# Optimization experiments

Measured on AMD Instinct MI355X. Metric: run time of the kernel, lower is better.

Reference implementation:

```python
import jax, jax.numpy as jnp
import numpy as np

B, L, D = 256, 256, 128          # batch, max_len, embedding_dim
H = W = 16                       # H=int(sqrt(L)), W=L//H
N, CBD = 128, 1024               # embedding_num, code_book_dim = N*8 = D*8
BETA = 0.25
BN_EPS = 1e-3                    # tf.layers.batch_normalization default


def _conv(x, w, b):
    return jax.lax.conv_general_dilated(x, w, (1, 1), 'VALID',
        dimension_numbers=('NHWC', 'HWIO', 'NHWC')) + b


def _convT(x, w, b):
    return jax.lax.conv_transpose(x, w, (1, 1), 'VALID',
        dimension_numbers=('NHWC', 'HWIO', 'NHWC')) + b


def _bn(x, g, b):
    # inference-mode BN with moving_mean=0, moving_var=1 (tf.layers default training=False)
    return g * (x * (1.0 / np.sqrt(1.0 + BN_EPS))) + b


def setup_inputs() -> dict:
    key = jax.random.key(0)
    ks = jax.random.split(key, 24)
    rn = lambda k, s, sc=0.05: (jax.random.normal(k, s, dtype=jnp.float32) * sc)
    inp = {
        'x': jax.random.normal(ks[0], (B, L, D), dtype=jnp.float32),
        'mask': jnp.ones((B, L), dtype=jnp.float32),
        'code_book': jax.random.normal(ks[1], (N, CBD), dtype=jnp.float32),
        # encoder: conv2d k=2 valid, channels D -> 2D -> 4D -> 8D
        'ew1': rn(ks[2], (2, 2, D, 2 * D)), 'eb1': jnp.zeros((2 * D,), jnp.float32),
        'eg1': jnp.ones((2 * D,), jnp.float32), 'ebt1': jnp.zeros((2 * D,), jnp.float32),
        'ew2': rn(ks[3], (2, 2, 2 * D, 4 * D)), 'eb2': jnp.zeros((4 * D,), jnp.float32),
        'eg2': jnp.ones((4 * D,), jnp.float32), 'ebt2': jnp.zeros((4 * D,), jnp.float32),
        'ew3': rn(ks[4], (2, 2, 4 * D, 8 * D)), 'eb3': jnp.zeros((8 * D,), jnp.float32),
        # decoder: conv2d_transpose k=2 valid, channels 8D -> 4D -> 2D -> D
        'dw1': rn(ks[5], (2, 2, 8 * D, 4 * D)), 'db1': jnp.zeros((4 * D,), jnp.float32),
        'dg1': jnp.ones((4 * D,), jnp.float32), 'dbt1': jnp.zeros((4 * D,), jnp.float32),
        'dw2': rn(ks[6], (2, 2, 4 * D, 2 * D)), 'db2': jnp.zeros((2 * D,), jnp.float32),
        'dg2': jnp.ones((2 * D,), jnp.float32), 'dbt2': jnp.zeros((2 * D,), jnp.float32),
        'dw3': rn(ks[7], (2, 2, 2 * D, D)), 'db3': jnp.zeros((D,), jnp.float32),
    }
    return inp


def reference(x, mask, code_book,
              ew1, eb1, eg1, ebt1, ew2, eb2, eg2, ebt2, ew3, eb3,
              dw1, db1, dg1, dbt1, dw2, db2, dg2, dbt2, dw3, db3):
    # ---- encoder (conv branch) ----
    xi = x.reshape(-1, H, W, D)                                   # [B,16,16,D]
    h = jax.nn.relu(_bn(_conv(xi, ew1, eb1), eg1, ebt1))          # [B,15,15,2D]
    h = jax.nn.relu(_bn(_conv(h, ew2, eb2), eg2, ebt2))           # [B,14,14,4D]
    x_encode = _conv(h, ew3, eb3)                                 # [B,13,13,8D]

    # ---- VQ codebook lookup (get_quantized) ----
    flat = x_encode.reshape(-1, CBD)                              # [B*169, CBD]
    dist = (jnp.sum(flat ** 2, axis=1, keepdims=True)
            + jnp.sum(code_book ** 2, axis=1)
            - 2.0 * flat @ code_book.T)                           # [B*169, N]
    idx = jnp.argmin(dist, axis=1)
    quantized = code_book[idx].reshape(x_encode.shape)            # gather == one_hot @ code_book

    # ---- straight-through + decoder ----
    ste = x_encode + jax.lax.stop_gradient(quantized - x_encode)
    h = jax.nn.relu(_bn(_convT(ste, dw1, db1), dg1, dbt1))        # [B,14,14,4D]
    h = jax.nn.relu(_bn(_convT(h, dw2, db2), dg2, dbt2))          # [B,15,15,2D]
    vq = _convT(h, dw3, db3)                                      # [B,16,16,D]
    vq_x = vq.reshape(-1, L, D)

    vq_mean = jnp.sum(vq_x, axis=1) / jnp.sum(mask, axis=-1, keepdims=True)

    recon = jnp.mean((x - vq_x) ** 2)
    vq_l = jnp.mean((quantized - jax.lax.stop_gradient(x_encode)) ** 2)
    commit = jnp.mean((x_encode - jax.lax.stop_gradient(quantized)) ** 2)
    vqvae_loss = recon + vq_l + BETA * commit
    return (vq_mean, vq_x, x_encode, quantized, vqvae_loss)
```

## Files before the change

kernel.cpp:

```cpp
#include <hip/hip_runtime.h>
#include <math.h>

typedef float f4 __attribute__((ext_vector_type(4)));
typedef short s8 __attribute__((ext_vector_type(8)));

#define WS_FLOATS 66000000L
__device__ float g_fallback[WS_FLOATS];

__device__ __forceinline__ f4 ldg4(const float* p) { return *(const f4*)p; }

__device__ __forceinline__ unsigned short bfr(float x) {
    unsigned int u = __float_as_uint(x);
    u += 0x7fffu + ((u >> 16) & 1u);
    return (unsigned short)(u >> 16);
}
__device__ __forceinline__ float bff(unsigned short h) {
    return __uint_as_float(((unsigned int)h) << 16);
}
__device__ __forceinline__ s8 z8() { s8 z = {0,0,0,0,0,0,0,0}; return z; }

__device__ __forceinline__ void split8(const f4& x0, const f4& x1, s8& hi, s8& lo) {
#pragma unroll
    for (int e = 0; e < 4; ++e) {
        unsigned short h0 = bfr(x0[e]);
        hi[e] = (short)h0; lo[e] = (short)bfr(x0[e] - bff(h0));
        unsigned short h1 = bfr(x1[e]);
        hi[e + 4] = (short)h1; lo[e + 4] = (short)bfr(x1[e] - bff(h1));
    }
}

template<int SPLIT, int ASRC, int EPI, int OUTF>
__global__ __launch_bounds__(256, 2)
void mfma_conv(const void* __restrict__ aHi, const void* __restrict__ aLo,
               const short* __restrict__ wHi, const short* __restrict__ wLo,
               const float* __restrict__ bias, const float* __restrict__ gamma,
               const float* __restrict__ beta,
               void* __restrict__ oHi, void* __restrict__ oLo,
               int* __restrict__ idxo,
               int IH, int IW, int Cin, int cinShift, int OHOW, int OW,
               int N, int K, int off, int ntShift, float bns)
{
    constexpr int PL = 128 * 64;
    __shared__ short smem[2 * SPLIT * PL];
    short* Ah = smem;
    short* Al = smem + PL;
    short* Bh = smem + SPLIT * PL;
    short* Bl = smem + SPLIT * PL + PL;

    const int tid = threadIdx.x;
    const int lane = tid & 63, wid = tid >> 6;
    const int fr = lane & 15, fq = lane >> 4;
    const int wm = (wid >> 1) * 64, wn = (wid & 1) * 64;

    int m0, n0;
    {
        const int nwg = gridDim.x;
        const int bid = blockIdx.x;
        const int q = nwg >> 3, r = nwg & 7;
        const int xcd = bid & 7, c = bid >> 3;
        const int wg = (xcd < r ? xcd * (q + 1) : r * (q + 1) + (xcd - r) * q) + c;
        const int NTm1 = (1 << ntShift) - 1;
        m0 = (wg >> ntShift) * 128;
        n0 = (wg & NTm1) * 128;
    }

    const int sr = tid >> 1;
    const int skh = (tid & 1) << 5;

    long tapOff[4]; bool tv[4];
    {
        int m = m0 + sr;
        int b = m / OHOW; int rem = m - b * OHOW;
        int oi = rem / OW; int oj = rem - oi * OW;
#pragma unroll
        for (int t = 0; t < 4; ++t) {
            int ii = oi + (t >> 1) + off, jj = oj + (t & 1) + off;
            bool v = (ii >= 0) && (ii < IH) && (jj >= 0) && (jj < IW);
            tv[t] = v;
            tapOff[t] = ((long)b * IH + (v ? ii : 0)) * IW + (v ? jj : 0);
        }
    }

    f4 acc[4][4];
#pragma unroll
    for (int a = 0; a < 4; ++a)
#pragma unroll
        for (int b = 0; b < 4; ++b) acc[a][b] = (f4){0.f, 0.f, 0.f, 0.f};

    const short* wHrow = wHi + (long)(n0 + sr) * K;
    const short* wLrow = (SPLIT == 2) ? (wLo + (long)(n0 + sr) * K) : nullptr;

    const int swzW = (sr & 7) << 3;
    const int sbase = sr * 64;

    s8 rah[4], ral[4], rbh[4], rbl[4];
    f4 rax0[4], rax1[4];

    auto LOADREGS = [&](int kc) {
        const int kk = kc + skh;
        const int t = kk >> cinShift;
        const int ci = kk & (Cin - 1);
        const bool v = tv[t];
        if (ASRC == 0) {
            const float* p = (const float*)aHi + tapOff[t] * Cin + ci;
#pragma unroll
            for (int q = 0; q < 4; ++q) {
                rax0[q] = v ? ldg4(p + 8 * q) : (f4){0.f,0.f,0.f,0.f};
                rax1[q] = v ? ldg4(p + 8 * q + 4) : (f4){0.f,0.f,0.f,0.f};
            }
        } else if (ASRC == 1) {
            const short* ph = (const short*)aHi + tapOff[t] * Cin + ci;
            const short* pl = (const short*)aLo + tapOff[t] * Cin + ci;
#pragma unroll
            for (int q = 0; q < 4; ++q) {
                rah[q] = v ? *(const s8*)(ph + 8 * q) : z8();
                ral[q] = v ? *(const s8*)(pl + 8 * q) : z8();
            }
        } else {
            const short* ph = (const short*)aHi + tapOff[t] * Cin + ci;
#pragma unroll
            for (int q = 0; q < 4; ++q) rah[q] = v ? *(const s8*)(ph + 8 * q) : z8();
        }
#pragma unroll
        for (int q = 0; q < 4; ++q) {
            rbh[q] = *(const s8*)(wHrow + kc + skh + 8 * q);
            if (SPLIT == 2) rbl[q] = *(const s8*)(wLrow + kc + skh + 8 * q);
        }
    };

    auto STORE = [&]() {
        if (ASRC == 0) {
#pragma unroll
            for (int q = 0; q < 4; ++q) split8(rax0[q], rax1[q], rah[q], ral[q]);
        }
#pragma unroll
        for (int q = 0; q < 4; ++q) {
            int kx = (skh + 8 * q) ^ swzW;
            *(s8*)&Ah[sbase + kx] = rah[q];
            if (SPLIT == 2) *(s8*)&Al[sbase + kx] = ral[q];
            *(s8*)&Bh[sbase + kx] = rbh[q];
            if (SPLIT == 2) *(s8*)&Bl[sbase + kx] = rbl[q];
        }
    };

    LOADREGS(0);
    for (int kc = 0; kc < K; kc += 64) {
        __syncthreads();
        STORE();
        __syncthreads();
        if (kc + 64 < K) LOADREGS(kc + 64);

        __builtin_amdgcn_s_setprio(1);
#pragma unroll
        for (int ks = 0; ks < 2; ++ks) {
            const int colk = ks * 32 + fq * 8;
            s8 afh[4], afl[4], bfh[4], bfl[4];
#pragma unroll
            for (int mf = 0; mf < 4; ++mf) {
                int ar = wm + mf * 16 + fr;
                int ai = ar * 64 + (colk ^ ((ar & 7) << 3));
                afh[mf] = *(const s8*)&Ah[ai];
                if (SPLIT == 2) afl[mf] = *(const s8*)&Al[ai];
            }
#pragma unroll
            for (int nf = 0; nf < 4; ++nf) {
                int br = wn + nf * 16 + fr;
                int bi2 = br * 64 + (colk ^ ((br & 7) << 3));
                bfh[nf] = *(const s8*)&Bh[bi2];
                if (SPLIT == 2) bfl[nf] = *(const s8*)&Bl[bi2];
            }
#pragma unroll
            for (int mf = 0; mf < 4; ++mf)
#pragma unroll
                for (int nf = 0; nf < 4; ++nf) {
                    acc[mf][nf] = __builtin_amdgcn_mfma_f32_16x16x32_bf16(
                        afh[mf], bfh[nf], acc[mf][nf], 0, 0, 0);
                    if (SPLIT == 2) {
                        acc[mf][nf] = __builtin_amdgcn_mfma_f32_16x16x32_bf16(
                            afh[mf], bfl[nf], acc[mf][nf], 0, 0, 0);
                        acc[mf][nf] = __builtin_amdgcn_mfma_f32_16x16x32_bf16(
                            afl[mf], bfh[nf], acc[mf][nf], 0, 0, 0);
                    }
                }
        }
        __builtin_amdgcn_s_setprio(0);
    }

    if (EPI == 2) {
        __syncthreads();
        float* pbv = (float*)smem;
        int*   piv = (int*)((float*)smem + 256);
        float cnv[4];
#pragma unroll
        for (int nf = 0; nf < 4; ++nf) cnv[nf] = bias[n0 + wn + nf * 16 + fr];
#pragma unroll
        for (int mf = 0; mf < 4; ++mf)
#pragma unroll
            for (int j = 0; j < 4; ++j) {
                float best = 3.4e38f; int bi = 0;
#pragma unroll
                for (int nf = 0; nf < 4; ++nf) {
                    float d = cnv[nf] - 2.0f * acc[mf][nf][j];
                    int col = wn + nf * 16 + fr;
                    if (d < best) { best = d; bi = col; }
                }
#pragma unroll
                for (int sh = 1; sh <= 8; sh <<= 1) {
                    float ov = __shfl_xor(best, sh, 64);
                    int ob = __shfl_xor(bi, sh, 64);
                    if (ov < best || (ov == best && ob < bi)) { best = ov; bi = ob; }
                }
                if (fr == 0) {
                    int r = wm + mf * 16 + fq * 4 + j;
                    pbv[(wid & 1) * 128 + r] = best;
                    piv[(wid & 1) * 128 + r] = bi;
                }
            }
        __syncthreads();
        if (tid < 128) {
            float b0 = pbv[tid], b1 = pbv[128 + tid];
            int i0 = piv[tid], i1 = piv[128 + tid];
            idxo[m0 + tid] = (b1 < b0) ? i1 : i0;
        }
        return;
    }

    float bi[4], ga[4], be[4];
#pragma unroll
    for (int nf = 0; nf < 4; ++nf) {
        int col = n0 + wn + nf * 16 + fr;
        bi[nf] = bias[col];
        if (EPI == 1) { ga[nf] = gamma[col]; be[nf] = beta[col]; }
    }
#pragma unroll
    for (int mf = 0; mf < 4; ++mf)
#pragma unroll
        for (int j = 0; j < 4; ++j) {
            long gm = m0 + wm + mf * 16 + fq * 4 + j;
#pragma unroll
            for (int nf = 0; nf < 4; ++nf) {
                int col = n0 + wn + nf * 16 + fr;
                float vv = acc[mf][nf][j] + bi[nf];
                if (EPI == 1) {
                    vv = ga[nf] * (vv * bns) + be[nf];
                    vv = fmaxf(vv, 0.f);
                }
                long o = gm * (long)N + col;
                if (OUTF == 0) {
                    ((float*)oHi)[o] = vv;
                } else if (OUTF == 2) {
                    ((short*)oHi)[o] = (short)bfr(vv);
                } else {
                    unsigned short h = bfr(vv);
                    ((short*)oHi)[o] = (short)h;
                    ((short*)oLo)[o] = (short)bfr(vv - bff(h));
                }
            }
        }
}

__global__ void prep_all(const float* __restrict__ ew1, const float* __restrict__ ew2,
                         const float* __restrict__ ew3, const float* __restrict__ dw1,
                         const float* __restrict__ dw2, const float* __restrict__ dw3,
                         const float* __restrict__ cb,
                         short* __restrict__ ewt1h, short* __restrict__ ewt1l,
                         short* __restrict__ ewt2h, short* __restrict__ ewt2l,
                         short* __restrict__ ewt3h,
                         short* __restrict__ dwt1Th, short* __restrict__ dwt1Tl,
                         short* __restrict__ dwt2h, short* __restrict__ dwt3h,
                         short* __restrict__ cbh, short* __restrict__ cbl,
                         float* __restrict__ zbuf)
{
    int b = blockIdx.x;
    int t = threadIdx.x;
    if (b < 512) {
        int i = b * 256 + t; int n = i >> 9, k = i & 511;
        float x = ew1[(long)k * 256 + n]; unsigned short h = bfr(x);
        ewt1h[i] = (short)h; ewt1l[i] = (short)bfr(x - bff(h));
    } else if (b < 2560) {
        int i = (b - 512) * 256 + t; int n = i >> 10, k = i & 1023;
        float x = ew2[(long)k * 512 + n]; unsigned short h = bfr(x);
        ewt2h[i] = (short)h; ewt2l[i] = (short)bfr(x - bff(h));
    } else if (b < 10752) {
        int i = (b - 2560) * 256 + t; int n = i >> 11, k = i & 2047;
        ewt3h[i] = (short)bfr(ew3[(long)k * 1024 + n]);
    } else if (b < 18944) {
        int i = (b - 10752) * 256 + t; int Np = i >> 10, co = i & 1023;
        int tt = Np >> 9, nn = Np & 511;
        float x = dw1[((long)(tt * 1024 + co)) * 512 + nn]; unsigned short h = bfr(x);
        dwt1Th[i] = (short)h; dwt1Tl[i] = (short)bfr(x - bff(h));
    } else if (b < 20992) {
        int i = (b - 18944) * 256 + t; int n = i >> 11, k = i & 2047;
        dwt2h[i] = (short)bfr(dw2[(long)k * 256 + n]);
    } else if (b < 21504) {
        int i = (b - 20992) * 256 + t; int n = i >> 10, k = i & 1023;
        dwt3h[i] = (short)bfr(dw3[(long)k * 128 + n]);
    } else if (b < 22016) {
        int i = (b - 21504) * 256 + t;
        float x = cb[i]; unsigned short h = bfr(x);
        cbh[i] = (short)h; cbl[i] = (short)bfr(x - bff(h));
    } else {
        int i = (b - 22016) * 256 + t; if (i < 2048) zbuf[i] = 0.f;
    }
}

__global__ void wsplitT(const float* __restrict__ p1, short* __restrict__ hi,
                        short* __restrict__ lo)
{
    int i = blockIdx.x * 256 + threadIdx.x;
    if (i >= 262144) return;
    int n = i >> 11, k = i & 2047;
    float x = p1[(long)k * 128 + n];
    unsigned short h = bfr(x);
    hi[i] = (short)h;
    lo[i] = (short)bfr(x - bff(h));
}

__global__ void code_bias(const float* __restrict__ cb, const float* __restrict__ eb3,
                          float* __restrict__ bias2)
{
    int c = blockIdx.x * 4 + (threadIdx.x >> 6);
    int lane = threadIdx.x & 63;
    if (c >= 128) return;
    const f4* p = (const f4*)(cb + (long)c * 1024);
    const f4* e = (const f4*)eb3;
    float s2 = 0.f, su = 0.f;
#pragma unroll
    for (int q = 0; q < 4; ++q) {
        f4 v = p[q * 64 + lane];
        f4 w = e[q * 64 + lane];
        s2 += (v[0]*v[0] + v[1]*v[1]) + (v[2]*v[2] + v[3]*v[3]);
        su += (v[0]*w[0] + v[1]*w[1]) + (v[2]*w[2] + v[3]*w[3]);
    }
#pragma unroll
    for (int sh = 32; sh; sh >>= 1) {
        s2 += __shfl_xor(s2, sh, 64);
        su += __shfl_xor(su, sh, 64);
    }
    if (lane == 0) bias2[c] = s2 - 2.f * su;
}

__global__ __launch_bounds__(256)
void d1_gather(const float* __restrict__ CD, const int* __restrict__ idx,
               const float* __restrict__ db1, const float* __restrict__ dg1,
               const float* __restrict__ dbt1, short* __restrict__ out, float bns)
{
    int m = blockIdx.x * 4 + (threadIdx.x >> 6);
    int lane = threadIdx.x & 63;
    if (m >= 50176) return;
    int b = m / 196, rem = m - b * 196;
    int oi = rem / 14, oj = rem - oi * 14;
    float2 acc[4];
#pragma unroll
    for (int q = 0; q < 4; ++q) acc[q] = make_float2(0.f, 0.f);
#pragma unroll
    for (int t = 0; t < 4; ++t) {
        int ii = oi - 1 + (t >> 1), jj = oj - 1 + (t & 1);
        if (ii >= 0 && ii < 13 && jj >= 0 && jj < 13) {
            int c = idx[(b * 13 + ii) * 13 + jj];
            const float2* p = (const float2*)(CD + ((long)c * 2048 + t * 512));
#pragma unroll
            for (int q = 0; q < 4; ++q) {
                float2 v = p[lane + 64 * q];
                acc[q].x += v.x; acc[q].y += v.y;
            }
        }
    }
#pragma unroll
    for (int q = 0; q < 4; ++q) {
        int n = 2 * (lane + 64 * q);
        float v0 = fmaxf(dg1[n]     * ((acc[q].x + db1[n])     * bns) + dbt1[n],     0.f);
        float v1 = fmaxf(dg1[n + 1] * ((acc[q].y + db1[n + 1]) * bns) + dbt1[n + 1], 0.f);
        short2 s2v;
        s2v.x = (short)bfr(v0); s2v.y = (short)bfr(v1);
        ((short2*)out)[(long)m * 256 + lane + 64 * q] = s2v;
    }
}

__global__ __launch_bounds__(256)
void gather_sq(const float* __restrict__ cb, const int* __restrict__ idx,
               const float* __restrict__ xe, float* __restrict__ q,
               double* __restrict__ part, int rows)
{
    __shared__ double red[256];
    double s = 0.0;
    for (int m = blockIdx.x; m < rows; m += gridDim.x) {
        int c = idx[m];
        const f4* src = (const f4*)(cb + (long)c * 1024);
        const f4* xs  = (const f4*)(xe + (long)m * 1024);
        f4* dst = (f4*)(q + (long)m * 1024);
        f4 v = src[threadIdx.x];
        f4 xv = xs[threadIdx.x];
        dst[threadIdx.x] = v;
        f4 d = v - xv;
        s += ((double)d[0]*d[0] + (double)d[1]*d[1]) + ((double)d[2]*d[2] + (double)d[3]*d[3]);
    }
    red[threadIdx.x] = s; __syncthreads();
    for (int h = 128; h; h >>= 1) {
        if (threadIdx.x < h) red[threadIdx.x] += red[threadIdx.x + h];
        __syncthreads();
    }
    if (threadIdx.x == 0) part[blockIdx.x] = red[0];
}

__global__ void sqdiff_partial(const float* __restrict__ a, const float* __restrict__ b,
                               double* __restrict__ part, long n4)
{
    __shared__ double red[256];
    long i = (long)blockIdx.x * blockDim.x + threadIdx.x;
    long stride = (long)gridDim.x * blockDim.x;
    const f4* A = (const f4*)a;
    const f4* B = (const f4*)b;
    f4 s = (f4){0.f, 0.f, 0.f, 0.f};
    for (; i < n4; i += stride) {
        f4 d = A[i] - B[i];
        s += d * d;
    }
    double t = ((double)s[0] + s[1]) + ((double)s[2] + s[3]);
    red[threadIdx.x] = t;
    __syncthreads();
    for (int h = 128; h; h >>= 1) {
        if (threadIdx.x < h) red[threadIdx.x] += red[threadIdx.x + h];
        __syncthreads();
    }
    if (threadIdx.x == 0) part[blockIdx.x] = red[0];
}

__global__ void finalize_k(const double* __restrict__ pa, int na,
                           const double* __restrict__ pb, int nb,
                           float* __restrict__ loss)
{
    __shared__ double red[256];
    int t = threadIdx.x;
    double sa = 0;
    for (int i = t; i < na; i += 256) sa += pa[i];
    red[t] = sa; __syncthreads();
    for (int h = 128; h; h >>= 1) { if (t < h) red[t] += red[t + h]; __syncthreads(); }
    double SA = red[0];
    __syncthreads();
    double sb = 0;
    for (int i = t; i < nb; i += 256) sb += pb[i];
    red[t] = sb; __syncthreads();
    for (int h = 128; h; h >>= 1) { if (t < h) red[t] += red[t + h]; __syncthreads(); }
    if (t == 0) {
        double recon = SA / 8388608.0;
        double vql = red[0] / 44302336.0;
        loss[0] = (float)(recon + 1.25 * vql);
    }
}

__global__ void vq_mean_k(const float* __restrict__ vqx, const float* __restrict__ mask,
                          float* __restrict__ o)
{
    __shared__ float red[128];
    int b = blockIdx.x;
    int d = threadIdx.x;
    red[d] = mask[b * 256 + d] + mask[b * 256 + 128 + d];
    __syncthreads();
    for (int h = 64; h; h >>= 1) { if (d < h) red[d] += red[d + h]; __syncthreads(); }
    float msum = red[0];
    const float* p = vqx + (long)b * 256 * 128 + d;
    float s = 0.f;
    for (int l = 0; l < 256; ++l) s += p[l * 128];
    o[b * 128 + d] = s / msum;
}

extern "C" void kernel_launch(void* const* d_in, const int* in_sizes, int n_in,
                              void* d_out, int out_size, void* d_ws, size_t ws_size,
                              hipStream_t stream)
{
    const float* x    = (const float*)d_in[0];
    const float* mask = (const float*)d_in[1];
    const float* cb   = (const float*)d_in[2];
    const float* ew1 = (const float*)d_in[3];
    const float* eb1 = (const float*)d_in[4];
    const float* eg1 = (const float*)d_in[5];
    const float* ebt1= (const float*)d_in[6];
    const float* ew2 = (const float*)d_in[7];
    const float* eb2 = (const float*)d_in[8];
    const float* eg2 = (const float*)d_in[9];
    const float* ebt2= (const float*)d_in[10];
    const float* ew3 = (const float*)d_in[11];
    const float* eb3 = (const float*)d_in[12];
    const float* dw1 = (const float*)d_in[13];
    const float* db1 = (const float*)d_in[14];
    const float* dg1 = (const float*)d_in[15];
    const float* dbt1= (const float*)d_in[16];
    const float* dw2 = (const float*)d_in[17];
    const float* db2 = (const float*)d_in[18];
    const float* dg2 = (const float*)d_in[19];
    const float* dbt2= (const float*)d_in[20];
    const float* dw3 = (const float*)d_in[21];
    const float* db3 = (const float*)d_in[22];

    float* out = (float*)d_out;
    float* o_vqmean = out;
    float* o_vqx    = out + 32768;
    float* o_xe     = out + 8421376;
    float* o_q      = out + 52723712;
    float* o_loss   = out + 97026048;

    float* base;
    if (ws_size >= (size_t)WS_FLOATS * 4) {
        base = (float*)d_ws;
    } else {
        void* p = nullptr;
        hipGetSymbolAddress(&p, HIP_SYMBOL(g_fallback));
        base = (float*)p;
    }

    float* cur = base;
    short* h1h = (short*)cur; cur += 7372800;
    short* h1l = (short*)cur; cur += 7372800;
    short* h2h = (short*)cur; cur += 12845056;
    short* h2l = (short*)cur; cur += 12845056;
    short* d1o = (short*)cur; cur += 12845056;
    short* d2o = (short*)cur; cur += 7372800;
    short* ewt1h = (short*)cur; cur += 65536;
    short* ewt1l = (short*)cur; cur += 65536;
    short* ewt2h = (short*)cur; cur += 262144;
    short* ewt2l = (short*)cur; cur += 262144;
    short* ewt3h = (short*)cur; cur += 1048576;
    short* dwt1Th = (short*)cur; cur += 1048576;
    short* dwt1Tl = (short*)cur; cur += 1048576;
    short* dwt2h = (short*)cur; cur += 262144;
    short* dwt3h = (short*)cur; cur += 65536;
    short* cbh   = (short*)cur; cur += 65536;
    short* cbl   = (short*)cur; cur += 65536;
    float* P1raw = cur; cur += 262144;
    short* wvh   = (short*)cur; cur += 131072;
    short* wvl   = (short*)cur; cur += 131072;
    float* CDt   = cur; cur += 262144;
    float* bias2 = cur; cur += 128;
    float* zbuf  = cur; cur += 2048;
    int* idxb = (int*)cur; cur += 43264;
    double* pa = (double*)cur; cur += 4096;
    double* pq = (double*)cur; cur += 4096;

    const float bns = (float)(1.0 / sqrt(1.0 + 1e-3));

    prep_all<<<22024, 256, 0, stream>>>(ew1, ew2, ew3, dw1, dw2, dw3, cb,
        ewt1h, ewt1l, ewt2h, ewt2l, ewt3h, dwt1Th, dwt1Tl, dwt2h, dwt3h,
        cbh, cbl, zbuf);
    code_bias<<<32, 256, 0, stream>>>(cb, eb3, bias2);

    mfma_conv<2, 0, 0, 0><<<16, 256, 0, stream>>>(
        ew3, nullptr, cbh, cbl, zbuf, nullptr, nullptr, P1raw, nullptr, nullptr,
        2, 2050, 1024, 10, 2048, 2048, 128, 1024, 0, 0, bns);
    wsplitT<<<1024, 256, 0, stream>>>(P1raw, wvh, wvl);
    mfma_conv<2, 0, 0, 0><<<16, 256, 0, stream>>>(
        cb, nullptr, dwt1Th, dwt1Tl, zbuf, nullptr, nullptr, CDt, nullptr, nullptr,
        2, 130, 1024, 10, 128, 128, 2048, 1024, 0, 4, bns);

    mfma_conv<2, 0, 1, 1><<<900, 256, 0, stream>>>(
        x, nullptr, ewt1h, ewt1l, eb1, eg1, ebt1, h1h, h1l, nullptr,
        16, 16, 128, 7, 225, 15, 256, 512, 0, 1, bns);
    mfma_conv<2, 1, 1, 1><<<1568, 256, 0, stream>>>(
        h1h, h1l, ewt2h, ewt2l, eb2, eg2, ebt2, h2h, h2l, nullptr,
        15, 15, 256, 8, 196, 14, 512, 1024, 0, 2, bns);
    mfma_conv<1, 2, 0, 0><<<2704, 256, 0, stream>>>(
        h2h, nullptr, ewt3h, nullptr, eb3, nullptr, nullptr, o_xe, nullptr, nullptr,
        14, 14, 512, 9, 169, 13, 1024, 2048, 0, 3, bns);

    mfma_conv<2, 1, 2, 0><<<338, 256, 0, stream>>>(
        h2h, h2l, wvh, wvl, bias2, nullptr, nullptr, nullptr, nullptr, idxb,
        14, 14, 512, 9, 169, 13, 128, 2048, 0, 0, bns);
    gather_sq<<<2048, 256, 0, stream>>>(cb, idxb, o_xe, o_q, pq, 43264);

    d1_gather<<<12544, 256, 0, stream>>>(CDt, idxb, db1, dg1, dbt1, d1o, bns);
    mfma_conv<1, 2, 1, 2><<<900, 256, 0, stream>>>(
        d1o, nullptr, dwt2h, nullptr, db2, dg2, dbt2, d2o, nullptr, nullptr,
        14, 14, 512, 9, 225, 15, 256, 2048, -1, 1, bns);
    mfma_conv<1, 2, 0, 0><<<512, 256, 0, stream>>>(
        d2o, nullptr, dwt3h, nullptr, db3, nullptr, nullptr, o_vqx, nullptr, nullptr,
        15, 15, 256, 8, 256, 16, 128, 1024, -1, 0, bns);

    vq_mean_k<<<256, 128, 0, stream>>>(o_vqx, mask, o_vqmean);
    sqdiff_partial<<<1024, 256, 0, stream>>>(x, o_vqx, pa, 2097152L);
    finalize_k<<<1, 256, 0, stream>>>(pa, 1024, pq, 2048, o_loss);
}
```

Measured before the change: 953.9 us.

## Fuse loss reductions into conv epilogues and stream B tiles via global_load_lds

In the SPLIT==1 conv path, the B-tile weights are now loaded straight into double-buffered LDS with global_load_lds and explicit waitcnt/barriers, so they no longer pass through registers. The squared-difference loss, the vq loss (using the argmin distance plus the ||x||^2 sum from the x_encode epilogue) and the vq_mean column sums are computed inside the conv epilogues with atomics. This removes the separate gather_sq, sqdiff_partial and vq_mean passes over large tensors. The cost is atomic contention and a nondeterministic floating-point summation order, and the vq loss is now rebuilt algebraically from distances, which can lose precision through cancellation.

```diff
diff --git a/kernel.cpp b/kernel.cpp
--- a/kernel.cpp
+++ b/kernel.cpp
@@ -37,15 +37,18 @@
                const float* __restrict__ beta,
                void* __restrict__ oHi, void* __restrict__ oLo,
                int* __restrict__ idxo,
+               const float* __restrict__ xref, float* __restrict__ colsum,
+               double* __restrict__ sacc,
                int IH, int IW, int Cin, int cinShift, int OHOW, int OW,
                int N, int K, int off, int ntShift, float bns)
 {
     constexpr int PL = 128 * 64;
-    __shared__ short smem[2 * SPLIT * PL];
+    constexpr int NPL = (SPLIT == 1) ? 3 : 4;
+    __shared__ short smem[NPL * PL];
     short* Ah = smem;
-    short* Al = smem + PL;
-    short* Bh = smem + SPLIT * PL;
-    short* Bl = smem + SPLIT * PL + PL;
+    short* Al  = smem + PL;
+    short* BhS = smem + 2 * PL;
+    short* BlS = smem + 3 * PL;
 
     const int tid = threadIdx.x;
     const int lane = tid & 63, wid = tid >> 6;
@@ -121,10 +124,12 @@
 #pragma unroll
             for (int q = 0; q < 4; ++q) rah[q] = v ? *(const s8*)(ph + 8 * q) : z8();
         }
-#pragma unroll
-        for (int q = 0; q < 4; ++q) {
-            rbh[q] = *(const s8*)(wHrow + kc + skh + 8 * q);
-            if (SPLIT == 2) rbl[q] = *(const s8*)(wLrow + kc + skh + 8 * q);
+        if (SPLIT == 2) {
+#pragma unroll
+            for (int q = 0; q < 4; ++q) {
+                rbh[q] = *(const s8*)(wHrow + kc + skh + 8 * q);
+                rbl[q] = *(const s8*)(wLrow + kc + skh + 8 * q);
+            }
         }
     };
 
@@ -137,18 +142,55 @@
         for (int q = 0; q < 4; ++q) {
             int kx = (skh + 8 * q) ^ swzW;
             *(s8*)&Ah[sbase + kx] = rah[q];
-            if (SPLIT == 2) *(s8*)&Al[sbase + kx] = ral[q];
-            *(s8*)&Bh[sbase + kx] = rbh[q];
-            if (SPLIT == 2) *(s8*)&Bl[sbase + kx] = rbl[q];
+            if (SPLIT == 2) {
+                *(s8*)&Al[sbase + kx]  = ral[q];
+                *(s8*)&BhS[sbase + kx] = rbh[q];
+                *(s8*)&BlS[sbase + kx] = rbl[q];
+            }
         }
     };
 
+    auto stageB = [&](int bsel, int kc2) {
+        short* bb = smem + (1 + bsel) * PL;
+        const int rr0 = wid << 5;
+#pragma unroll
+        for (int i = 0; i < 4; ++i) {
+            const int r = rr0 + 8 * i + (lane >> 3);
+            const int c = lane & 7;
+            const short* src = wHi + (long)(n0 + r) * K + kc2 + 8 * (c ^ (r & 7));
+            __builtin_amdgcn_global_load_lds(
+                (const __attribute__((address_space(1))) void*)src,
+                (__attribute__((address_space(3))) void*)(bb + (rr0 + 8 * i) * 64),
+                16, 0, 0);
+        }
+    };
+
+    int bcur = 0;
     LOADREGS(0);
+    if (SPLIT == 1) stageB(0, 0);
+
     for (int kc = 0; kc < K; kc += 64) {
-        __syncthreads();
-        STORE();
-        __syncthreads();
+        if (SPLIT == 1) {
+            asm volatile("s_waitcnt lgkmcnt(0)" ::: "memory");
+            __builtin_amdgcn_s_barrier();
+            STORE();
+            if (kc + 64 < K) {
+                stageB(bcur ^ 1, kc + 64);
+                asm volatile("s_waitcnt vmcnt(4)" ::: "memory");
+            } else {
+                asm volatile("s_waitcnt vmcnt(0)" ::: "memory");
+            }
+            __builtin_amdgcn_sched_barrier(0);
+            asm volatile("s_waitcnt lgkmcnt(0)" ::: "memory");
+            __builtin_amdgcn_s_barrier();
+        } else {
+            __syncthreads();
+            STORE();
+            __syncthreads();
+        }
         if (kc + 64 < K) LOADREGS(kc + 64);
+
+        const short* Bc = (SPLIT == 1) ? (smem + (1 + bcur) * PL) : BhS;
 
         __builtin_amdgcn_s_setprio(1);
 #pragma unroll
@@ -166,8 +208,8 @@
             for (int nf = 0; nf < 4; ++nf) {
                 int br = wn + nf * 16 + fr;
                 int bi2 = br * 64 + (colk ^ ((br & 7) << 3));
-                bfh[nf] = *(const s8*)&Bh[bi2];
-                if (SPLIT == 2) bfl[nf] = *(const s8*)&Bl[bi2];
+                bfh[nf] = *(const s8*)&Bc[bi2];
+                if (SPLIT == 2) bfl[nf] = *(const s8*)&BlS[bi2];
             }
 #pragma unroll
             for (int mf = 0; mf < 4; ++mf)
@@ -184,6 +226,7 @@
                 }
         }
         __builtin_amdgcn_s_setprio(0);
+        bcur ^= 1;
     }
 
     if (EPI == 2) {
@@ -217,11 +260,21 @@
                 }
             }
         __syncthreads();
+        double win = 0.0;
         if (tid < 128) {
             float b0 = pbv[tid], b1 = pbv[128 + tid];
             int i0 = piv[tid], i1 = piv[128 + tid];
             idxo[m0 + tid] = (b1 < b0) ? i1 : i0;
-        }
+            win = (double)((b1 < b0) ? b1 : b0);
+        }
+        __syncthreads();
+        double* rd = (double*)smem;
+        rd[tid] = win; __syncthreads();
+        for (int h = 128; h; h >>= 1) {
+            if (tid < h) rd[tid] += rd[tid + h];
+            __syncthreads();
+        }
+        if (tid == 0) atomicAdd(sacc, rd[0]);
         return;
     }
 
@@ -232,6 +285,8 @@
         bi[nf] = bias[col];
         if (EPI == 1) { ga[nf] = gamma[col]; be[nf] = beta[col]; }
     }
+    double tsum = 0.0;
+    float csum[4] = {0.f, 0.f, 0.f, 0.f};
 #pragma unroll
     for (int mf = 0; mf < 4; ++mf)
 #pragma unroll
@@ -255,8 +310,30 @@
                     ((short*)oHi)[o] = (short)h;
                     ((short*)oLo)[o] = (short)bfr(vv - bff(h));
                 }
-            }
-        }
+                if (EPI == 3) tsum += (double)vv * vv;
+                if (EPI == 4) {
+                    float d = vv - xref[o];
+                    tsum += (double)d * d;
+                    csum[nf] += vv;
+                }
+            }
+        }
+    if (EPI == 4) {
+        int bb128 = (m0 >> 8) * 128;
+#pragma unroll
+        for (int nf = 0; nf < 4; ++nf)
+            atomicAdd(&colsum[bb128 + n0 + wn + nf * 16 + fr], csum[nf]);
+    }
+    if (EPI == 3 || EPI == 4) {
+        __syncthreads();
+        double* rd = (double*)smem;
+        rd[tid] = tsum; __syncthreads();
+        for (int h = 128; h; h >>= 1) {
+            if (tid < h) rd[tid] += rd[tid + h];
+            __syncthreads();
+        }
+        if (tid == 0) atomicAdd(sacc, rd[0]);
+    }
 }
 
 __global__ void prep_all(const float* __restrict__ ew1, const float* __restrict__ ew2,
@@ -377,80 +454,24 @@
     }
 }
 
-__global__ __launch_bounds__(256)
-void gather_sq(const float* __restrict__ cb, const int* __restrict__ idx,
-               const float* __restrict__ xe, float* __restrict__ q,
-               double* __restrict__ part, int rows)
-{
-    __shared__ double red[256];
-    double s = 0.0;
-    for (int m = blockIdx.x; m < rows; m += gridDim.x) {
-        int c = idx[m];
-        const f4* src = (const f4*)(cb + (long)c * 1024);
-        const f4* xs  = (const f4*)(xe + (long)m * 1024);
-        f4* dst = (f4*)(q + (long)m * 1024);
-        f4 v = src[threadIdx.x];
-        f4 xv = xs[threadIdx.x];
-        dst[threadIdx.x] = v;
-        f4 d = v - xv;
-        s += ((double)d[0]*d[0] + (double)d[1]*d[1]) + ((double)d[2]*d[2] + (double)d[3]*d[3]);
-    }
-    red[threadIdx.x] = s; __syncthreads();
-    for (int h = 128; h; h >>= 1) {
-        if (threadIdx.x < h) red[threadIdx.x] += red[threadIdx.x + h];
-        __syncthreads();
-    }
-    if (threadIdx.x == 0) part[blockIdx.x] = red[0];
-}
-
-__global__ void sqdiff_partial(const float* __restrict__ a, const float* __restrict__ b,
-                               double* __restrict__ part, long n4)
-{
-    __shared__ double red[256];
-    long i = (long)blockIdx.x * blockDim.x + threadIdx.x;
-    long stride = (long)gridDim.x * blockDim.x;
-    const f4* A = (const f4*)a;
-    const f4* B = (const f4*)b;
-    f4 s = (f4){0.f, 0.f, 0.f, 0.f};
-    for (; i < n4; i += stride) {
-        f4 d = A[i] - B[i];
-        s += d * d;
-    }
-    double t = ((double)s[0] + s[1]) + ((double)s[2] + s[3]);
-    red[threadIdx.x] = t;
-    __syncthreads();
-    for (int h = 128; h; h >>= 1) {
-        if (threadIdx.x < h) red[threadIdx.x] += red[threadIdx.x + h];
-        __syncthreads();
-    }
-    if (threadIdx.x == 0) part[blockIdx.x] = red[0];
-}
-
-__global__ void finalize_k(const double* __restrict__ pa, int na,
-                           const double* __restrict__ pb, int nb,
-                           float* __restrict__ loss)
-{
-    __shared__ double red[256];
-    int t = threadIdx.x;
-    double sa = 0;
-    for (int i = t; i < na; i += 256) sa += pa[i];
-    red[t] = sa; __syncthreads();
-    for (int h = 128; h; h >>= 1) { if (t < h) red[t] += red[t + h]; __syncthreads(); }
-    double SA = red[0];
-    __syncthreads();
-    double sb = 0;
-    for (int i = t; i < nb; i += 256) sb += pb[i];
-    red[t] = sb; __syncthreads();
-    for (int h = 128; h; h >>= 1) { if (t < h) red[t] += red[t + h]; __syncthreads(); }
-    if (t == 0) {
-        double recon = SA / 8388608.0;
-        double vql = red[0] / 44302336.0;
-        loss[0] = (float)(recon + 1.25 * vql);
-    }
-}
-
-__global__ void vq_mean_k(const float* __restrict__ vqx, const float* __restrict__ mask,
-                          float* __restrict__ o)
+__global__ void gather_rows(const float* __restrict__ cb, const int* __restrict__ idx,
+                            float* __restrict__ q)
+{
+    int m = blockIdx.x;
+    int c = idx[m];
+    const f4* src = (const f4*)(cb + (long)c * 1024);
+    f4* dst = (f4*)(q + (long)m * 1024);
+    dst[threadIdx.x] = src[threadIdx.x];
+}
+
+__global__ void finalize2(const double* __restrict__ s, float* __restrict__ loss)
+{
+    if (threadIdx.x == 0)
+        loss[0] = (float)(s[0] / 8388608.0 + 1.25 * ((s[1] + s[2]) / 44302336.0));
+}
+
+__global__ void vq_mean_fin(const float* __restrict__ colsum,
+                            const float* __restrict__ mask, float* __restrict__ o)
 {
     __shared__ float red[128];
     int b = blockIdx.x;
@@ -458,11 +479,7 @@
     red[d] = mask[b * 256 + d] + mask[b * 256 + 128 + d];
     __syncthreads();
     for (int h = 64; h; h >>= 1) { if (d < h) red[d] += red[d + h]; __syncthreads(); }
-    float msum = red[0];
-    const float* p = vqx + (long)b * 256 * 128 + d;
-    float s = 0.f;
-    for (int l = 0; l < 256; ++l) s += p[l * 128];
-    o[b * 128 + d] = s / msum;
+    o[b * 128 + d] = colsum[b * 128 + d] / red[0];
 }
 
 extern "C" void kernel_launch(void* const* d_in, const int* in_sizes, int n_in,
@@ -534,11 +551,13 @@
     float* bias2 = cur; cur += 128;
     float* zbuf  = cur; cur += 2048;
     int* idxb = (int*)cur; cur += 43264;
-    double* pa = (double*)cur; cur += 4096;
-    double* pq = (double*)cur; cur += 4096;
+    float* colsum = cur; cur += 32768;
+    double* sdbl = (double*)cur; cur += 16;
 
     const float bns = (float)(1.0 / sqrt(1.0 + 1e-3));
 
+    hipMemsetAsync(colsum, 0, 32768 * sizeof(float), stream);
+    hipMemsetAsync(sdbl, 0, 3 * sizeof(double), stream);
     prep_all<<<22024, 256, 0, stream>>>(ew1, ew2, ew3, dw1, dw2, dw3, cb,
         ewt1h, ewt1l, ewt2h, ewt2l, ewt3h, dwt1Th, dwt1Tl, dwt2h, dwt3h,
         cbh, cbl, zbuf);
@@ -546,36 +565,43 @@
 
     mfma_conv<2, 0, 0, 0><<<16, 256, 0, stream>>>(
         ew3, nullptr, cbh, cbl, zbuf, nullptr, nullptr, P1raw, nullptr, nullptr,
+        nullptr, nullptr, nullptr,
         2, 2050, 1024, 10, 2048, 2048, 128, 1024, 0, 0, bns);
     wsplitT<<<1024, 256, 0, stream>>>(P1raw, wvh, wvl);
     mfma_conv<2, 0, 0, 0><<<16, 256, 0, stream>>>(
         cb, nullptr, dwt1Th, dwt1Tl, zbuf, nullptr, nullptr, CDt, nullptr, nullptr,
+        nullptr, nullptr, nullptr,
         2, 130, 1024, 10, 128, 128, 2048, 1024, 0, 4, bns);
 
     mfma_conv<2, 0, 1, 1><<<900, 256, 0, stream>>>(
         x, nullptr, ewt1h, ewt1l, eb1, eg1, ebt1, h1h, h1l, nullptr,
+        nullptr, nullptr, nullptr,
         16, 16, 128, 7, 225, 15, 256, 512, 0, 1, bns);
     mfma_conv<2, 1, 1, 1><<<1568, 256, 0, stream>>>(
         h1h, h1l, ewt2h, ewt2l, eb2, eg2, ebt2, h2h, h2l, nullptr,
+        nullptr, nullptr, nullptr,
         15, 15, 256, 8, 196, 14, 512, 1024, 0, 2, bns);
-    mfma_conv<1, 2, 0, 0><<<2704, 256, 0, stream>>>(
+    mfma_conv<1, 2, 3, 0><<<2704, 256, 0, stream>>>(
         h2h, nullptr, ewt3h, nullptr, eb3, nullptr, nullptr, o_xe, nullptr, nullptr,
+        nullptr, nullptr, sdbl + 1,
         14, 14, 512, 9, 169, 13, 1024, 2048, 0, 3, bns);
 
     mfma_conv<2, 1, 2, 0><<<338, 256, 0, stream>>>(
         h2h, h2l, wvh, wvl, bias2, nullptr, nullptr, nullptr, nullptr, idxb,
+        nullptr, nullptr, sdbl + 2,
         14, 14, 512, 9, 169, 13, 128, 2048, 0, 0, bns);
-    gather_sq<<<2048, 256, 0, stream>>>(cb, idxb, o_xe, o_q, pq, 43264);
+    gather_rows<<<43264, 256, 0, stream>>>(cb, idxb, o_q);
 
     d1_gather<<<12544, 256, 0, stream>>>(CDt, idxb, db1, dg1, dbt1, d1o, bns);
     mfma_conv<1, 2, 1, 2><<<900, 256, 0, stream>>>(
         d1o, nullptr, dwt2h, nullptr, db2, dg2, dbt2, d2o, nullptr, nullptr,
+        nullptr, nullptr, nullptr,
         14, 14, 512, 9, 225, 15, 256, 2048, -1, 1, bns);
-    mfma_conv<1, 2, 0, 0><<<512, 256, 0, stream>>>(
+    mfma_conv<1, 2, 4, 0><<<512, 256, 0, stream>>>(
         d2o, nullptr, dwt3h, nullptr, db3, nullptr, nullptr, o_vqx, nullptr, nullptr,
+        x, colsum, sdbl + 0,
         15, 15, 256, 8, 256, 16, 128, 1024, -1, 0, bns);
 
-    vq_mean_k<<<256, 128, 0, stream>>>(o_vqx, mask, o_vqmean);
-    sqdiff_partial<<<1024, 256, 0, stream>>>(x, o_vqx, pa, 2097152L);
-    finalize_k<<<1, 256, 0, stream>>>(pa, 1024, pq, 2048, o_loss);
-}
+    vq_mean_fin<<<256, 128, 0, stream>>>(colsum, mask, o_vqmean);
+    finalize2<<<1, 64, 0, stream>>>(sdbl, o_loss);
+}
```

After: 912.3 us. 1.05x faster.
